# Optimization experiments

Measured on AMD Instinct MI355X. Metric: run time of the kernel, lower is better.

Reference implementation:

```python
import jax, jax.numpy as jnp
import numpy as np

EPS = 1.1920929e-07  # float32 eps, matches torch.finfo(torch.float32).eps
QMAX = 127.0         # 2**(8-1)-1 for 8-bit symmetric quantization
NUM_HEADS = 12


def _round_ste(x):
    return x + jax.lax.stop_gradient(jnp.round(x) - x)


def _floor_ste(x):
    return x + jax.lax.stop_gradient(jnp.floor(x) - x)


def _act_quant(x):
    # per-tensor symmetric 8-bit (QuantAct + SymmetricQuantFunction)
    s = jax.lax.stop_gradient(jnp.maximum(jnp.max(jnp.abs(x)) / QMAX, EPS))
    return jnp.clip(_round_ste(x / s), -QMAX - 1.0, QMAX), s


def _weight_quant(w):
    # per-output-channel symmetric 8-bit (scale.view(-1,1) path in linear_quantize)
    s = jax.lax.stop_gradient(jnp.maximum(jnp.max(jnp.abs(w), axis=1) / QMAX, EPS))
    return jnp.clip(_round_ste(w / s[:, None]), -QMAX - 1.0, QMAX), s


def _fixedpoint_requant(pre_act, pre_s, z_s):
    # fixedpoint_mul: requantize int accumulator (value pre_act on scale pre_s)
    # onto scale z_s using a 31-bit mantissa/exponent decomposition (batch_frexp).
    def int_path(pa):
        z_int = jnp.round(pa / pre_s)
        ns = pre_s / z_s
        e = jnp.floor(jnp.log2(ns)) + 1.0          # frexp exponent: ns = m * 2**e, m in [0.5,1)
        m = jnp.floor(ns * jnp.exp2(-e) * 2.0 ** 31 + 0.5)  # ROUND_HALF_UP mantissa * 2**31
        out = jnp.round(z_int * m * jnp.exp2(e - 31.0))
        return jnp.clip(out, -QMAX - 1.0, QMAX)
    hard = jax.lax.stop_gradient(int_path(pre_act))
    soft = pre_act / z_s                            # STE backward: grad / z_scaling_factor
    return soft + jax.lax.stop_gradient(hard - soft)


def _int_softmax(x_int, sf, output_bit=8, n=15):
    # IntSoftmax (shiftmax) with int_exp_shift; x_int = logits / sf (integer-valued)
    x_int = x_int - jnp.max(x_int, axis=-1, keepdims=True)
    x_int = x_int + _floor_ste(x_int / 2.0) - _floor_ste(x_int / 16.0)
    x0 = jax.lax.stop_gradient(jnp.floor(-1.0 / sf))
    x_int = jnp.maximum(x_int, n * x0)
    q = _floor_ste(x_int / x0)
    r = x_int - x0 * q
    exp_int = jnp.clip(_floor_ste((r / 2.0 - x0) * jnp.exp2(n - q)), 0.0, None)
    esum = jnp.minimum(jnp.sum(exp_int, axis=-1, keepdims=True), 2.0 ** 31 - 1.0)
    factor = _floor_ste((2.0 ** 31 - 1.0) / esum)
    exp_int = _floor_ste(exp_int * factor / 2.0 ** (31 - output_bit + 1))
    return exp_int, 1.0 / 2.0 ** (output_bit - 1)


def setup_inputs() -> dict:
    key = jax.random.key(0)
    k1, k2, k3, k4, k5 = jax.random.split(key, 5)
    B, N, C = 8, 577, 768
    return {
        "x": jax.random.normal(k1, (B, N, C), dtype=jnp.float32),
        "w_qkv": jax.random.normal(k2, (3 * C, C), dtype=jnp.float32) * 0.02,
        "b_qkv": jax.random.normal(k3, (3 * C,), dtype=jnp.float32) * 0.01,
        "w_proj": jax.random.normal(k4, (C, C), dtype=jnp.float32) * 0.02,
        "b_proj": jax.random.normal(k5, (C,), dtype=jnp.float32) * 0.01,
    }


def reference(x, w_qkv, b_qkv, w_proj, b_proj):
    B, N, C = x.shape
    H = NUM_HEADS
    D = C // H
    # ---- quantize input activation and qkv weight, integer GEMM ----
    x_int, s_x = _act_quant(x)                         # [B,N,C] int-valued, scalar scale
    wq_int, s_wq = _weight_quant(w_qkv)                # [3C,C], per-channel scale [3C]
    acc_s = s_x * s_wq                                 # accumulator scale [3C]
    qkv_int = jnp.einsum('bnc,oc->bno', x_int, wq_int) + _round_ste(b_qkv / acc_s)
    qkv_f = qkv_int * acc_s                            # dequantized qkv [B,N,3C]
    # ---- requantize qkv to per-tensor 8-bit via fixed-point mul ----
    s_qkv = jax.lax.stop_gradient(jnp.maximum(jnp.max(jnp.abs(qkv_f)) / QMAX, EPS))
    qkv8 = _fixedpoint_requant(qkv_f, acc_s, s_qkv)    # int8-valued [B,N,3C]
    qkv8 = qkv8.reshape(B, N, 3, H, D).transpose(2, 0, 3, 1, 4)
    q, k, v = qkv8[0], qkv8[1], qkv8[2]                # each [B,H,N,D]
    # ---- integer attention logits; float scale carries head_dim**-0.5 ----
    attn_int = jnp.einsum('bhnd,bhmd->bhnm', q, k)
    s_attn = s_qkv * s_qkv * (D ** -0.5)
    sm_int, s_sm = _int_softmax(attn_int, s_attn)      # int probs on scale 1/128
    # ---- integer attn @ v ----
    ctx_int = jnp.einsum('bhnm,bhmd->bhnd', sm_int, v)
    ctx_f = (ctx_int * (s_sm * s_qkv)).transpose(0, 2, 1, 3).reshape(B, N, C)
    s_ctx = jax.lax.stop_gradient(jnp.maximum(jnp.max(jnp.abs(ctx_f)) / QMAX, EPS))
    ctx8 = _fixedpoint_requant(ctx_f, s_sm * s_qkv, s_ctx)
    # ---- quantized output projection ----
    wp_int, s_wp = _weight_quant(w_proj)
    out_s = s_ctx * s_wp
    out_int = jnp.einsum('bnc,oc->bno', ctx8, wp_int) + _round_ste(b_proj / out_s)
    return out_int * out_s
```

## Files before the change

### kernel.cpp

```cpp
#include <hip/hip_runtime.h>
#include <math.h>

#define BQ 8
#define SEQ 577
#define CH 768
#define NH 12
#define HD 64
#define M_ROWS (BQ * SEQ)
#define QKV_CH (3 * CH)
#define NX (M_ROWS * CH)
#define EPSF 1.1920929e-07f
#define F2P31 2147483648.0f

#define VT_ROW 640
#define P_STRIDE 664

typedef __attribute__((ext_vector_type(4))) int i32x4;
typedef struct __align__(16) { long x, y; } L2T;

__device__ __forceinline__ void mfma_gemm_core_lds(
    const signed char* __restrict__ A, const signed char* __restrict__ Bm,
    signed char* As, signed char* Bs,
    int arow0, int bcol0, int w, int lane, i32x4 acc[4][4]) {
  int c = lane & 15, q = lane >> 4;
  int lr = lane >> 2;
  int ksb = (lane & 3) << 4;
  const signed char* Aw = As + ((w & 1) << 12);
  const signed char* Bw = Bs + ((w >> 1) << 12);
  for (int k0 = 0; k0 < CH; k0 += 64) {
#pragma unroll
    for (int u = 0; u < 2; ++u) {
      int row = (w << 5) + (u << 4) + lr;
      __builtin_amdgcn_global_load_lds(
          (const __attribute__((address_space(1))) void*)(A + (size_t)(arow0 + row) * CH + k0 + ksb),
          (__attribute__((address_space(3))) void*)(As + (w << 11) + (u << 10)),
          16, 0, 0);
      __builtin_amdgcn_global_load_lds(
          (const __attribute__((address_space(1))) void*)(Bm + (size_t)(bcol0 + row) * CH + k0 + ksb),
          (__attribute__((address_space(3))) void*)(Bs + (w << 11) + (u << 10)),
          16, 0, 0);
    }
    __syncthreads();
    L2T af[4], bf[4];
#pragma unroll
    for (int i = 0; i < 4; ++i)
      af[i] = *(const L2T*)(Aw + (((i << 4) + c) << 6) + (q << 4));
#pragma unroll
    for (int j = 0; j < 4; ++j)
      bf[j] = *(const L2T*)(Bw + (((j << 4) + c) << 6) + (q << 4));
#pragma unroll
    for (int i = 0; i < 4; ++i)
#pragma unroll
      for (int j = 0; j < 4; ++j) {
        acc[i][j] = __builtin_amdgcn_mfma_i32_16x16x32_i8(af[i].x, bf[j].x, acc[i][j], 0, 0, 0);
        acc[i][j] = __builtin_amdgcn_mfma_i32_16x16x32_i8(af[i].y, bf[j].y, acc[i][j], 0, 0, 0);
      }
    __syncthreads();
  }
}

__global__ __launch_bounds__(256) void k_prep(
    const float* __restrict__ x, const float* __restrict__ w_qkv,
    const float* __restrict__ w_proj,
    signed char* __restrict__ WQ8, float* __restrict__ SWQ,
    signed char* __restrict__ WP8, float* __restrict__ SWP,
    unsigned* __restrict__ gmax) {
  __shared__ float red[4];
  int blk = blockIdx.x, tid = threadIdx.x;
  if (blk < QKV_CH + CH) {
    const float* wr; signed char* w8; float* sw; int r;
    if (blk < QKV_CH) { r = blk; wr = w_qkv + (size_t)r * CH; w8 = WQ8 + (size_t)r * CH; sw = SWQ; }
    else { r = blk - QKV_CH; wr = w_proj + (size_t)r * CH; w8 = WP8 + (size_t)r * CH; sw = SWP; }
    float m = 0.f;
    for (int c = tid; c < CH; c += 256) m = fmaxf(m, fabsf(wr[c]));
#pragma unroll
    for (int o = 32; o; o >>= 1) m = fmaxf(m, __shfl_xor(m, o, 64));
    if ((tid & 63) == 0) red[tid >> 6] = m;
    __syncthreads();
    float mm = fmaxf(fmaxf(red[0], red[1]), fmaxf(red[2], red[3]));
    float s = fmaxf(mm / 127.0f, EPSF);
    if (tid == 0) sw[r] = s;
    for (int c = tid; c < CH; c += 256) {
      float q = rintf(wr[c] / s);
      q = fminf(fmaxf(q, -128.f), 127.f);
      w8[c] = (signed char)q;
    }
  } else {
    int ab = blk - (QKV_CH + CH);
    const float4* x4 = (const float4*)x;
    float m = 0.f;
    for (int i = ab * 256 + tid; i < NX / 4; i += 1024 * 256) {
      float4 v = x4[i];
      m = fmaxf(m, fmaxf(fmaxf(fabsf(v.x), fabsf(v.y)), fmaxf(fabsf(v.z), fabsf(v.w))));
    }
#pragma unroll
    for (int o = 32; o; o >>= 1) m = fmaxf(m, __shfl_xor(m, o, 64));
    if ((tid & 63) == 0) red[tid >> 6] = m;
    __syncthreads();
    if (tid == 0)
      atomicMax(gmax, __float_as_uint(fmaxf(fmaxf(red[0], red[1]), fmaxf(red[2], red[3]))));
  }
}

__global__ void k_aquant(const float* __restrict__ x, int n,
                         const unsigned* __restrict__ hdr, signed char* __restrict__ x8) {
  float s = fmaxf(__uint_as_float(hdr[0]) / 127.0f, EPSF);
  int n4 = n >> 2;
  const float4* x4 = (const float4*)x;
  int* dst = (int*)x8;
  int stride = gridDim.x * blockDim.x;
  for (int i = blockIdx.x * blockDim.x + threadIdx.x; i < n4; i += stride) {
    float4 v = x4[i];
    int pk = 0;
#pragma unroll
    for (int u = 0; u < 4; ++u) {
      float xv = (u == 0) ? v.x : (u == 1) ? v.y : (u == 2) ? v.z : v.w;
      float q = rintf(xv / s);
      q = fminf(fmaxf(q, -128.f), 127.f);
      pk |= ((int)(signed char)q & 0xff) << (u * 8);
    }
    dst[i] = pk;
  }
}

__global__ __launch_bounds__(256) void k_gemm_qkv(
    const signed char* __restrict__ A, const signed char* __restrict__ Bm,
    const float* __restrict__ swq, const float* __restrict__ bias,
    const unsigned* __restrict__ hdr, int* __restrict__ Cq, unsigned* __restrict__ gq) {
  __shared__ signed char As[8192], Bs[8192];
  __shared__ float red[4];
  int t = threadIdx.x;
  int lane = t & 63, w = t >> 6;
  int c = lane & 15, q = lane >> 4;
  int arow = blockIdx.y * 128 + (w & 1) * 64;
  int bcol = blockIdx.x * 128 + (w >> 1) * 64;
  i32x4 acc[4][4] = {};
  mfma_gemm_core_lds(A, Bm, As, Bs, blockIdx.y * 128, blockIdx.x * 128, w, lane, acc);
  float s_x = fmaxf(__uint_as_float(hdr[0]) / 127.0f, EPSF);
  float lmax = 0.f;
#pragma unroll
  for (int j = 0; j < 4; ++j) {
    int ccol = bcol + j * 16 + c;
    float accs = s_x * swq[ccol];
    int bint = (int)rintf(bias[ccol] / accs);
#pragma unroll
    for (int i = 0; i < 4; ++i)
#pragma unroll
      for (int r = 0; r < 4; ++r) {
        int rr = arow + i * 16 + q * 4 + r;
        if (rr < M_ROWS) {
          int qv = acc[i][j][r] + bint;
          Cq[(size_t)rr * QKV_CH + ccol] = qv;
          lmax = fmaxf(lmax, fabsf((float)qv * accs));
        }
      }
  }
#pragma unroll
  for (int off = 32; off; off >>= 1) lmax = fmaxf(lmax, __shfl_xor(lmax, off, 64));
  if (lane == 0) red[w] = lmax;
  __syncthreads();
  if (t == 0)
    atomicMax(gq, __float_as_uint(fmaxf(fmaxf(red[0], red[1]), fmaxf(red[2], red[3]))));
}

#define QK_BLKS 870
__global__ __launch_bounds__(256) void k_qkv_requant(
    const int* __restrict__ Cq, const float* __restrict__ swq,
    const unsigned* __restrict__ hdr,
    signed char* __restrict__ Q8, signed char* __restrict__ K8,
    signed char* __restrict__ VT8) {
  float s_x = fmaxf(__uint_as_float(hdr[0]) / 127.0f, EPSF);
  float s_qkv = fmaxf(__uint_as_float(hdr[1]) / 127.0f, EPSF);
  int blk = blockIdx.x, tid = threadIdx.x;
  if (blk < QK_BLKS) {
    int bx = blk % 6, by = blk / 6;
    int o = bx * 256 + tid;
    float accs = s_x * swq[o];
    float ns = accs / s_qkv;
    int e; float f = frexpf(ns, &e);
    float mm = floorf(f * F2P31 + 0.5f);
    float pw = __int_as_float((e + 96) << 23);
    int isK = (o >= CH);
    int rem = o - (isK ? CH : 0);
    int h = rem >> 6, d = rem & 63;
    signed char* dstb = isK ? K8 : Q8;
    int bn0 = by * 32;
    int bnend = min(bn0 + 32, M_ROWS);
    for (int bn = bn0; bn < bnend; ++bn) {
      int qv = Cq[(size_t)bn * QKV_CH + o];
      float qf = (float)qv * accs;
      float z = rintf(qf / accs);
      float t8 = rintf((z * mm) * pw);
      t8 = fminf(fmaxf(t8, -128.f), 127.f);
      int b = bn / SEQ, n = bn - b * SEQ;
      dstb[(((size_t)(b * NH + h) * SEQ + n) << 6) + d] = (signed char)t8;
    }
  } else {
    __shared__ signed char VTt[64 * 68];
    int vt = blk - QK_BLKS;
    int bh = vt / 10, n0 = (vt - bh * 10) * 64;
    int b = bh / NH, h = bh - b * NH;
    int od = tid & 63;
    int o = 2 * CH + h * 64 + od;
    float accs = s_x * swq[o];
    float ns = accs / s_qkv;
    int e; float f = frexpf(ns, &e);
    float mm = floorf(f * F2P31 + 0.5f);
    float pw = __int_as_float((e + 96) << 23);
    int nr = tid >> 6;
    for (int p = 0; p < 16; ++p) {
      int nl = nr * 16 + p;
      int n = n0 + nl;
      signed char v = 0;
      if (n < SEQ) {
        int qv = Cq[(size_t)(b * SEQ + n) * QKV_CH + o];
        float qf = (float)qv * accs;
        float z = rintf(qf / accs);
        float t8 = rintf((z * mm) * pw);
        t8 = fminf(fmaxf(t8, -128.f), 127.f);
        v = (signed char)t8;
      }
      VTt[od * 68 + nl] = v;
    }
    __syncthreads();
    int w16 = tid & 15, dr = tid >> 4;
#pragma unroll
    for (int pp = 0; pp < 4; ++pp) {
      int d = pp * 16 + dr;
      int val = *(const int*)&VTt[d * 68 + w16 * 4];
      *(int*)(VT8 + (size_t)bh * (64 * VT_ROW) + (size_t)d * VT_ROW + n0 + w16 * 4) = val;
    }
  }
}

__global__ __launch_bounds__(256, 4) void k_attn(
    const signed char* __restrict__ Q8, const signed char* __restrict__ K8,
    const signed char* __restrict__ VT8, const unsigned* __restrict__ hdr,
    int* __restrict__ ctxi, unsigned* __restrict__ gctx) {
  __shared__ unsigned char P[16 * P_STRIDE];
  __shared__ int Rmax[4][16];
  __shared__ unsigned long long Rsum[4][16];
  __shared__ float Rav[4];
  int tid = threadIdx.x;
  int t = tid & 63, wid = tid >> 6;
  int lin = blockIdx.x;
  int j = lin >> 3;
  int bh = (lin & 7) * 12 + j / 37;
  int qt = j % 37;
  int b = bh / NH, h = bh - b * NH;
  int col = t & 15, q4 = t >> 4;
  {
    int r = tid >> 4, w4 = tid & 15;
    *(int*)&P[r * P_STRIDE + 576 + (w4 << 2)] = 0;
  }
  const signed char* Qb = Q8 + (((size_t)bh * SEQ + qt * 16 + col) << 6);
  long qa0 = *(const long*)(Qb + q4 * 8);
  long qa1 = *(const long*)(Qb + 32 + q4 * 8);
  const signed char* Kb = K8 + ((size_t)bh * SEQ << 6);
  int kt0 = (wid == 0) ? 0 : 10 + (wid - 1) * 9;
  int ktn = (wid == 0) ? 10 : 9;
  i32x4 sv[10];
  int mx[4] = {-2147483647 - 1, -2147483647 - 1, -2147483647 - 1, -2147483647 - 1};
#pragma unroll
  for (int u = 0; u < 10; ++u) {
    if (u < ktn) {
      int kt = kt0 + u;
      const signed char* kr = Kb + ((size_t)(kt * 16 + col) << 6);
      long kb0 = *(const long*)(kr + q4 * 8);
      long kb1 = *(const long*)(kr + 32 + q4 * 8);
      i32x4 a = {0, 0, 0, 0};
      a = __builtin_amdgcn_mfma_i32_16x16x32_i8(qa0, kb0, a, 0, 0, 0);
      a = __builtin_amdgcn_mfma_i32_16x16x32_i8(qa1, kb1, a, 0, 0, 0);
      sv[u] = a;
      bool valid = (kt < 36) | (col < 1);
#pragma unroll
      for (int r = 0; r < 4; ++r)
        if (valid) mx[r] = max(mx[r], a[r]);
    }
  }
#pragma unroll
  for (int r = 0; r < 4; ++r) {
    mx[r] = max(mx[r], __shfl_xor(mx[r], 1, 64));
    mx[r] = max(mx[r], __shfl_xor(mx[r], 2, 64));
    mx[r] = max(mx[r], __shfl_xor(mx[r], 4, 64));
    mx[r] = max(mx[r], __shfl_xor(mx[r], 8, 64));
  }
  if (col == 0) {
#pragma unroll
    for (int r = 0; r < 4; ++r) Rmax[wid][q4 * 4 + r] = mx[r];
  }
  __syncthreads();
#pragma unroll
  for (int r = 0; r < 4; ++r) {
    int row = q4 * 4 + r;
    mx[r] = max(max(Rmax[0][row], Rmax[1][row]), max(Rmax[2][row], Rmax[3][row]));
  }
  float s_qkv = fmaxf(__uint_as_float(hdr[1]) / 127.0f, EPSF);
  float s_attn = (s_qkv * s_qkv) * 0.125f;
  float x0f = floorf(-1.0f / s_attn);
  int x0i = (int)x0f;
  int bi = -x0i;
  int nx0i = 15 * x0i;
  int twob = bi << 1;
  unsigned Mq = 0xFFFFFFFFu / (unsigned)bi + 1u;
  bool bOne = (Mq == 0u);
  unsigned long long su[4] = {0ull, 0ull, 0ull, 0ull};
#pragma unroll
  for (int u = 0; u < 10; ++u) {
    if (u < ktn) {
      int kt = kt0 + u;
      bool valid = (kt < 36) | (col < 1);
#pragma unroll
      for (int r = 0; r < 4; ++r) {
        int d = sv[u][r] - mx[r];
        int xi = d + (d >> 1) - (d >> 4);
        xi = max(xi, nx0i);
        xi = min(xi, 0);
        unsigned a = (unsigned)(-xi);
        unsigned q = bOne ? a : __umulhi(a, Mq);
        int rr = (int)(a - q * (unsigned)bi);
        unsigned m = (unsigned)(twob - rr);
        unsigned ue = (q < 15u) ? (m << (14 - q)) : (m >> 1);
        ue = valid ? ue : 0u;
        su[r] += ue;
        sv[u][r] = (int)ue;
      }
    }
  }
#pragma unroll
  for (int r = 0; r < 4; ++r) {
    su[r] += __shfl_xor(su[r], 1, 64);
    su[r] += __shfl_xor(su[r], 2, 64);
    su[r] += __shfl_xor(su[r], 4, 64);
    su[r] += __shfl_xor(su[r], 8, 64);
  }
  if (col == 0) {
#pragma unroll
    for (int r = 0; r < 4; ++r) Rsum[wid][q4 * 4 + r] = su[r];
  }
  __syncthreads();
  float fac[4];
#pragma unroll
  for (int r = 0; r < 4; ++r) {
    int row = q4 * 4 + r;
    unsigned long long dv = ((Rsum[0][row] + Rsum[1][row]) + Rsum[2][row]) + Rsum[3][row];
    float esum = fminf((float)dv, F2P31);
    fac[r] = floorf(F2P31 / esum);
  }
#pragma unroll
  for (int u = 0; u < 10; ++u) {
    if (u < ktn) {
      int kt = kt0 + u;
#pragma unroll
      for (int r = 0; r < 4; ++r) {
        float e = (float)(unsigned)sv[u][r];
        int p = (int)floorf((e * fac[r]) * 5.9604644775390625e-08f);
        P[(q4 * 4 + r) * P_STRIDE + kt * 16 + col] = (unsigned char)p;
      }
    }
  }
  __syncthreads();
  const signed char* Vb = VT8 + (size_t)bh * (64 * VT_ROW);
  i32x4 acc = {0, 0, 0, 0};
  for (int mc = 0; mc < 20; ++mc) {
    long pa = *(const long*)&P[col * P_STRIDE + mc * 32 + q4 * 8];
    long vb = *(const long*)(Vb + (size_t)(wid * 16 + col) * VT_ROW + mc * 32 + q4 * 8);
    acc = __builtin_amdgcn_mfma_i32_16x16x32_i8(pa, vb, acc, 0, 0, 0);
  }
  float pre_s = 0.0078125f * s_qkv;
  float avmax = 0.f;
#pragma unroll
  for (int r = 0; r < 4; ++r) {
    int n = qt * 16 + q4 * 4 + r;
    if (n < SEQ) {
      int cacc = acc[r];
      ctxi[((size_t)(b * SEQ + n)) * CH + h * 64 + wid * 16 + col] = cacc;
      avmax = fmaxf(avmax, fabsf((float)cacc * pre_s));
    }
  }
#pragma unroll
  for (int off = 32; off; off >>= 1) avmax = fmaxf(avmax, __shfl_xor(avmax, off, 64));
  if (t == 0) Rav[wid] = avmax;
  __syncthreads();
  if (tid == 0)
    atomicMax(gctx, __float_as_uint(fmaxf(fmaxf(Rav[0], Rav[1]), fmaxf(Rav[2], Rav[3]))));
}

__global__ void k_ctx_requant(const int* __restrict__ ctxi, const unsigned* __restrict__ hdr,
                              signed char* __restrict__ C8) {
  float s_qkv = fmaxf(__uint_as_float(hdr[1]) / 127.0f, EPSF);
  float pre_s = 0.0078125f * s_qkv;
  float s_ctx = fmaxf(__uint_as_float(hdr[2]) / 127.0f, EPSF);
  float ns = pre_s / s_ctx;
  int e;
  float f = frexpf(ns, &e);
  float mm = floorf(f * F2P31 + 0.5f);
  float pw = exp2f((float)e - 31.0f);
  int total4 = (M_ROWS * CH) / 4;
  int stride = gridDim.x * blockDim.x;
  const int4* src = (const int4*)ctxi;
  int* dst = (int*)C8;
  for (int i = blockIdx.x * blockDim.x + threadIdx.x; i < total4; i += stride) {
    int4 v = src[i];
    int pk = 0;
#pragma unroll
    for (int u = 0; u < 4; ++u) {
      int cv = (u == 0) ? v.x : (u == 1) ? v.y : (u == 2) ? v.z : v.w;
      float cf = (float)cv * pre_s;
      float z = rintf(cf / pre_s);
      float t8 = rintf((z * mm) * pw);
      t8 = fminf(fmaxf(t8, -128.f), 127.f);
      pk |= ((int)(signed char)t8 & 0xff) << (u * 8);
    }
    dst[i] = pk;
  }
}

__global__ __launch_bounds__(256) void k_gemm_out(
    const signed char* __restrict__ A, const signed char* __restrict__ Bm,
    const float* __restrict__ swp, const float* __restrict__ bias,
    const unsigned* __restrict__ hdr, float* __restrict__ outp) {
  __shared__ signed char As[8192], Bs[8192];
  int t = threadIdx.x;
  int lane = t & 63, w = t >> 6;
  int c = lane & 15, q = lane >> 4;
  int arow = blockIdx.y * 128 + (w & 1) * 64;
  int bcol = blockIdx.x * 128 + (w >> 1) * 64;
  i32x4 acc[4][4] = {};
  mfma_gemm_core_lds(A, Bm, As, Bs, blockIdx.y * 128, blockIdx.x * 128, w, lane, acc);
  float s_ctx = fmaxf(__uint_as_float(hdr[2]) / 127.0f, EPSF);
#pragma unroll
  for (int j = 0; j < 4; ++j) {
    int ccol = bcol + j * 16 + c;
    float outs = s_ctx * swp[ccol];
    int bint = (int)rintf(bias[ccol] / outs);
#pragma unroll
    for (int i = 0; i < 4; ++i)
#pragma unroll
      for (int r = 0; r < 4; ++r) {
        int rr = arow + i * 16 + q * 4 + r;
        if (rr < M_ROWS)
          outp[(size_t)rr * CH + ccol] = (float)(acc[i][j][r] + bint) * outs;
      }
  }
}

extern "C" void kernel_launch(void* const* d_in, const int* in_sizes, int n_in,
                              void* d_out, int out_size, void* d_ws, size_t ws_size,
                              hipStream_t stream) {
  const float* x = (const float*)d_in[0];
  const float* w_qkv = (const float*)d_in[1];
  const float* b_qkv = (const float*)d_in[2];
  const float* w_proj = (const float*)d_in[3];
  const float* b_proj = (const float*)d_in[4];
  float* outp = (float*)d_out;

  char* ws = (char*)d_ws;
  size_t off = 0;
  auto alloc = [&](size_t sz) -> char* {
    char* p = ws + off;
    off = (off + sz + 4095) & ~(size_t)4095;
    return p;
  };
  unsigned* hdr = (unsigned*)alloc(256);
  float* SWQ = (float*)alloc(QKV_CH * 4);
  float* SWP = (float*)alloc(CH * 4);
  signed char* WQ8 = (signed char*)alloc((size_t)QKV_CH * CH);
  signed char* WP8 = (signed char*)alloc((size_t)CH * CH);
  signed char* X8  = (signed char*)alloc((size_t)(M_ROWS + 128) * CH);
  signed char* Q8  = (signed char*)alloc((size_t)M_ROWS * CH);
  signed char* K8  = (signed char*)alloc((size_t)M_ROWS * CH);
  signed char* VT8 = (signed char*)alloc((size_t)BQ * NH * 64 * VT_ROW);
  signed char* C8  = (signed char*)alloc((size_t)(M_ROWS + 128) * CH);
  int* QKVI = (int*)alloc((size_t)M_ROWS * QKV_CH * 4);
  int* CTXI = (int*)alloc((size_t)M_ROWS * CH * 4);
  (void)ws_size;

  hipMemsetAsync(hdr, 0, 256, stream);
  k_prep<<<QKV_CH + CH + 1024, 256, 0, stream>>>(x, w_qkv, w_proj, WQ8, SWQ, WP8, SWP, hdr + 0);
  k_aquant<<<2048, 256, 0, stream>>>(x, NX, hdr, X8);
  dim3 g1(QKV_CH / 128, (M_ROWS + 127) / 128);
  k_gemm_qkv<<<g1, 256, 0, stream>>>(X8, WQ8, SWQ, b_qkv, hdr, QKVI, hdr + 1);
  k_qkv_requant<<<QK_BLKS + BQ * NH * 10, 256, 0, stream>>>(QKVI, SWQ, hdr, Q8, K8, VT8);
  k_attn<<<37 * BQ * NH, 256, 0, stream>>>(Q8, K8, VT8, hdr, CTXI, hdr + 2);
  k_ctx_requant<<<1024, 256, 0, stream>>>(CTXI, hdr, C8);
  dim3 g2(CH / 128, (M_ROWS + 127) / 128);
  k_gemm_out<<<g2, 256, 0, stream>>>(C8, WP8, SWP, b_proj, hdr, outp);
}
```

Before: 223.4 us.

## Use 16x16x64 int8 MFMA and spread global max atomics over slots

```diff
diff --git a/kernel.cpp b/kernel.cpp
--- a/kernel.cpp
+++ b/kernel.cpp
@@ -13,10 +13,19 @@
 #define F2P31 2147483648.0f
 
 #define VT_ROW 640
-#define P_STRIDE 664
+#define P_STRIDE 688
+
+#define NSLOT 64
+#define SLOT_STRIDE 16
 
 typedef __attribute__((ext_vector_type(4))) int i32x4;
-typedef struct __align__(16) { long x, y; } L2T;
+
+__device__ __forceinline__ float slot_scale(const unsigned* __restrict__ s) {
+  float m = 0.f;
+#pragma unroll
+  for (int i = 0; i < NSLOT; ++i) m = fmaxf(m, __uint_as_float(s[i * SLOT_STRIDE]));
+  return fmaxf(m * (1.0f / 127.0f) == 0.f ? 0.f : m / 127.0f, EPSF);
+}
 
 __device__ __forceinline__ void mfma_gemm_core_lds(
     const signed char* __restrict__ A, const signed char* __restrict__ Bm,
@@ -41,20 +50,18 @@
           16, 0, 0);
     }
     __syncthreads();
-    L2T af[4], bf[4];
+    i32x4 af[4], bf[4];
 #pragma unroll
     for (int i = 0; i < 4; ++i)
-      af[i] = *(const L2T*)(Aw + (((i << 4) + c) << 6) + (q << 4));
+      af[i] = *(const i32x4*)(Aw + (((i << 4) + c) << 6) + (q << 4));
 #pragma unroll
     for (int j = 0; j < 4; ++j)
-      bf[j] = *(const L2T*)(Bw + (((j << 4) + c) << 6) + (q << 4));
+      bf[j] = *(const i32x4*)(Bw + (((j << 4) + c) << 6) + (q << 4));
 #pragma unroll
     for (int i = 0; i < 4; ++i)
 #pragma unroll
-      for (int j = 0; j < 4; ++j) {
-        acc[i][j] = __builtin_amdgcn_mfma_i32_16x16x32_i8(af[i].x, bf[j].x, acc[i][j], 0, 0, 0);
-        acc[i][j] = __builtin_amdgcn_mfma_i32_16x16x32_i8(af[i].y, bf[j].y, acc[i][j], 0, 0, 0);
-      }
+      for (int j = 0; j < 4; ++j)
+        acc[i][j] = __builtin_amdgcn_mfma_i32_16x16x64_i8(af[i], bf[j], acc[i][j], 0, 0, 0);
     __syncthreads();
   }
 }
@@ -64,7 +71,7 @@
     const float* __restrict__ w_proj,
     signed char* __restrict__ WQ8, float* __restrict__ SWQ,
     signed char* __restrict__ WP8, float* __restrict__ SWP,
-    unsigned* __restrict__ gmax) {
+    unsigned* __restrict__ mxx) {
   __shared__ float red[4];
   int blk = blockIdx.x, tid = threadIdx.x;
   if (blk < QKV_CH + CH) {
@@ -98,13 +105,14 @@
     if ((tid & 63) == 0) red[tid >> 6] = m;
     __syncthreads();
     if (tid == 0)
-      atomicMax(gmax, __float_as_uint(fmaxf(fmaxf(red[0], red[1]), fmaxf(red[2], red[3]))));
+      atomicMax(&mxx[(ab & (NSLOT - 1)) * SLOT_STRIDE],
+                __float_as_uint(fmaxf(fmaxf(red[0], red[1]), fmaxf(red[2], red[3]))));
   }
 }
 
 __global__ void k_aquant(const float* __restrict__ x, int n,
-                         const unsigned* __restrict__ hdr, signed char* __restrict__ x8) {
-  float s = fmaxf(__uint_as_float(hdr[0]) / 127.0f, EPSF);
+                         const unsigned* __restrict__ mxx, signed char* __restrict__ x8) {
+  float s = slot_scale(mxx);
   int n4 = n >> 2;
   const float4* x4 = (const float4*)x;
   int* dst = (int*)x8;
@@ -126,7 +134,7 @@
 __global__ __launch_bounds__(256) void k_gemm_qkv(
     const signed char* __restrict__ A, const signed char* __restrict__ Bm,
     const float* __restrict__ swq, const float* __restrict__ bias,
-    const unsigned* __restrict__ hdr, int* __restrict__ Cq, unsigned* __restrict__ gq) {
+    const unsigned* __restrict__ mxx, int* __restrict__ Cq, unsigned* __restrict__ mxq) {
   __shared__ signed char As[8192], Bs[8192];
   __shared__ float red[4];
   int t = threadIdx.x;
@@ -136,7 +144,7 @@
   int bcol = blockIdx.x * 128 + (w >> 1) * 64;
   i32x4 acc[4][4] = {};
   mfma_gemm_core_lds(A, Bm, As, Bs, blockIdx.y * 128, blockIdx.x * 128, w, lane, acc);
-  float s_x = fmaxf(__uint_as_float(hdr[0]) / 127.0f, EPSF);
+  float s_x = slot_scale(mxx);
   float lmax = 0.f;
 #pragma unroll
   for (int j = 0; j < 4; ++j) {
@@ -160,17 +168,18 @@
   if (lane == 0) red[w] = lmax;
   __syncthreads();
   if (t == 0)
-    atomicMax(gq, __float_as_uint(fmaxf(fmaxf(red[0], red[1]), fmaxf(red[2], red[3]))));
+    atomicMax(&mxq[((blockIdx.y * 18 + blockIdx.x) & (NSLOT - 1)) * SLOT_STRIDE],
+              __float_as_uint(fmaxf(fmaxf(red[0], red[1]), fmaxf(red[2], red[3]))));
 }
 
 #define QK_BLKS 870
 __global__ __launch_bounds__(256) void k_qkv_requant(
     const int* __restrict__ Cq, const float* __restrict__ swq,
-    const unsigned* __restrict__ hdr,
+    const unsigned* __restrict__ mxx, const unsigned* __restrict__ mxq,
     signed char* __restrict__ Q8, signed char* __restrict__ K8,
     signed char* __restrict__ VT8) {
-  float s_x = fmaxf(__uint_as_float(hdr[0]) / 127.0f, EPSF);
-  float s_qkv = fmaxf(__uint_as_float(hdr[1]) / 127.0f, EPSF);
+  float s_x = slot_scale(mxx);
+  float s_qkv = slot_scale(mxq);
   int blk = blockIdx.x, tid = threadIdx.x;
   if (blk < QK_BLKS) {
     int bx = blk % 6, by = blk / 6;
@@ -235,8 +244,8 @@
 
 __global__ __launch_bounds__(256, 4) void k_attn(
     const signed char* __restrict__ Q8, const signed char* __restrict__ K8,
-    const signed char* __restrict__ VT8, const unsigned* __restrict__ hdr,
-    int* __restrict__ ctxi, unsigned* __restrict__ gctx) {
+    const signed char* __restrict__ VT8, const unsigned* __restrict__ mxq,
+    int* __restrict__ ctxi, unsigned* __restrict__ mxc) {
   __shared__ unsigned char P[16 * P_STRIDE];
   __shared__ int Rmax[4][16];
   __shared__ unsigned long long Rsum[4][16];
@@ -254,8 +263,7 @@
     *(int*)&P[r * P_STRIDE + 576 + (w4 << 2)] = 0;
   }
   const signed char* Qb = Q8 + (((size_t)bh * SEQ + qt * 16 + col) << 6);
-  long qa0 = *(const long*)(Qb + q4 * 8);
-  long qa1 = *(const long*)(Qb + 32 + q4 * 8);
+  i32x4 qa = *(const i32x4*)(Qb + q4 * 16);
   const signed char* Kb = K8 + ((size_t)bh * SEQ << 6);
   int kt0 = (wid == 0) ? 0 : 10 + (wid - 1) * 9;
   int ktn = (wid == 0) ? 10 : 9;
@@ -266,11 +274,9 @@
     if (u < ktn) {
       int kt = kt0 + u;
       const signed char* kr = Kb + ((size_t)(kt * 16 + col) << 6);
-      long kb0 = *(const long*)(kr + q4 * 8);
-      long kb1 = *(const long*)(kr + 32 + q4 * 8);
+      i32x4 kb = *(const i32x4*)(kr + q4 * 16);
       i32x4 a = {0, 0, 0, 0};
-      a = __builtin_amdgcn_mfma_i32_16x16x32_i8(qa0, kb0, a, 0, 0, 0);
-      a = __builtin_amdgcn_mfma_i32_16x16x32_i8(qa1, kb1, a, 0, 0, 0);
+      a = __builtin_amdgcn_mfma_i32_16x16x64_i8(qa, kb, a, 0, 0, 0);
       sv[u] = a;
       bool valid = (kt < 36) | (col < 1);
 #pragma unroll
@@ -295,7 +301,7 @@
     int row = q4 * 4 + r;
     mx[r] = max(max(Rmax[0][row], Rmax[1][row]), max(Rmax[2][row], Rmax[3][row]));
   }
-  float s_qkv = fmaxf(__uint_as_float(hdr[1]) / 127.0f, EPSF);
+  float s_qkv = slot_scale(mxq);
   float s_attn = (s_qkv * s_qkv) * 0.125f;
   float x0f = floorf(-1.0f / s_attn);
   int x0i = (int)x0f;
@@ -361,11 +367,15 @@
   }
   __syncthreads();
   const signed char* Vb = VT8 + (size_t)bh * (64 * VT_ROW);
-  i32x4 acc = {0, 0, 0, 0};
-  for (int mc = 0; mc < 20; ++mc) {
-    long pa = *(const long*)&P[col * P_STRIDE + mc * 32 + q4 * 8];
-    long vb = *(const long*)(Vb + (size_t)(wid * 16 + col) * VT_ROW + mc * 32 + q4 * 8);
-    acc = __builtin_amdgcn_mfma_i32_16x16x32_i8(pa, vb, acc, 0, 0, 0);
+  i32x4 ac0 = {0, 0, 0, 0}, ac1 = {0, 0, 0, 0};
+#pragma unroll
+  for (int mc = 0; mc < 10; mc += 2) {
+    i32x4 pa0 = *(const i32x4*)&P[col * P_STRIDE + mc * 64 + q4 * 16];
+    i32x4 vb0 = *(const i32x4*)(Vb + (size_t)(wid * 16 + col) * VT_ROW + mc * 64 + q4 * 16);
+    ac0 = __builtin_amdgcn_mfma_i32_16x16x64_i8(pa0, vb0, ac0, 0, 0, 0);
+    i32x4 pa1 = *(const i32x4*)&P[col * P_STRIDE + (mc + 1) * 64 + q4 * 16];
+    i32x4 vb1 = *(const i32x4*)(Vb + (size_t)(wid * 16 + col) * VT_ROW + (mc + 1) * 64 + q4 * 16);
+    ac1 = __builtin_amdgcn_mfma_i32_16x16x64_i8(pa1, vb1, ac1, 0, 0, 0);
   }
   float pre_s = 0.0078125f * s_qkv;
   float avmax = 0.f;
@@ -373,7 +383,7 @@
   for (int r = 0; r < 4; ++r) {
     int n = qt * 16 + q4 * 4 + r;
     if (n < SEQ) {
-      int cacc = acc[r];
+      int cacc = ac0[r] + ac1[r];
       ctxi[((size_t)(b * SEQ + n)) * CH + h * 64 + wid * 16 + col] = cacc;
       avmax = fmaxf(avmax, fabsf((float)cacc * pre_s));
     }
@@ -383,14 +393,15 @@
   if (t == 0) Rav[wid] = avmax;
   __syncthreads();
   if (tid == 0)
-    atomicMax(gctx, __float_as_uint(fmaxf(fmaxf(Rav[0], Rav[1]), fmaxf(Rav[2], Rav[3]))));
-}
-
-__global__ void k_ctx_requant(const int* __restrict__ ctxi, const unsigned* __restrict__ hdr,
-                              signed char* __restrict__ C8) {
-  float s_qkv = fmaxf(__uint_as_float(hdr[1]) / 127.0f, EPSF);
+    atomicMax(&mxc[(blockIdx.x & (NSLOT - 1)) * SLOT_STRIDE],
+              __float_as_uint(fmaxf(fmaxf(Rav[0], Rav[1]), fmaxf(Rav[2], Rav[3]))));
+}
+
+__global__ void k_ctx_requant(const int* __restrict__ ctxi, const unsigned* __restrict__ mxq,
+                              const unsigned* __restrict__ mxc, signed char* __restrict__ C8) {
+  float s_qkv = slot_scale(mxq);
   float pre_s = 0.0078125f * s_qkv;
-  float s_ctx = fmaxf(__uint_as_float(hdr[2]) / 127.0f, EPSF);
+  float s_ctx = slot_scale(mxc);
   float ns = pre_s / s_ctx;
   int e;
   float f = frexpf(ns, &e);
@@ -419,7 +430,7 @@
 __global__ __launch_bounds__(256) void k_gemm_out(
     const signed char* __restrict__ A, const signed char* __restrict__ Bm,
     const float* __restrict__ swp, const float* __restrict__ bias,
-    const unsigned* __restrict__ hdr, float* __restrict__ outp) {
+    const unsigned* __restrict__ mxc, float* __restrict__ outp) {
   __shared__ signed char As[8192], Bs[8192];
   int t = threadIdx.x;
   int lane = t & 63, w = t >> 6;
@@ -428,7 +439,7 @@
   int bcol = blockIdx.x * 128 + (w >> 1) * 64;
   i32x4 acc[4][4] = {};
   mfma_gemm_core_lds(A, Bm, As, Bs, blockIdx.y * 128, blockIdx.x * 128, w, lane, acc);
-  float s_ctx = fmaxf(__uint_as_float(hdr[2]) / 127.0f, EPSF);
+  float s_ctx = slot_scale(mxc);
 #pragma unroll
   for (int j = 0; j < 4; ++j) {
     int ccol = bcol + j * 16 + c;
@@ -462,7 +473,9 @@
     off = (off + sz + 4095) & ~(size_t)4095;
     return p;
   };
-  unsigned* hdr = (unsigned*)alloc(256);
+  unsigned* mxx = (unsigned*)alloc(3 * NSLOT * SLOT_STRIDE * 4);
+  unsigned* mxq = mxx + NSLOT * SLOT_STRIDE;
+  unsigned* mxc = mxq + NSLOT * SLOT_STRIDE;
   float* SWQ = (float*)alloc(QKV_CH * 4);
   float* SWP = (float*)alloc(CH * 4);
   signed char* WQ8 = (signed char*)alloc((size_t)QKV_CH * CH);
@@ -476,14 +489,14 @@
   int* CTXI = (int*)alloc((size_t)M_ROWS * CH * 4);
   (void)ws_size;
 
-  hipMemsetAsync(hdr, 0, 256, stream);
-  k_prep<<<QKV_CH + CH + 1024, 256, 0, stream>>>(x, w_qkv, w_proj, WQ8, SWQ, WP8, SWP, hdr + 0);
-  k_aquant<<<2048, 256, 0, stream>>>(x, NX, hdr, X8);
+  hipMemsetAsync(mxx, 0, 3 * NSLOT * SLOT_STRIDE * 4, stream);
+  k_prep<<<QKV_CH + CH + 1024, 256, 0, stream>>>(x, w_qkv, w_proj, WQ8, SWQ, WP8, SWP, mxx);
+  k_aquant<<<2048, 256, 0, stream>>>(x, NX, mxx, X8);
   dim3 g1(QKV_CH / 128, (M_ROWS + 127) / 128);
-  k_gemm_qkv<<<g1, 256, 0, stream>>>(X8, WQ8, SWQ, b_qkv, hdr, QKVI, hdr + 1);
-  k_qkv_requant<<<QK_BLKS + BQ * NH * 10, 256, 0, stream>>>(QKVI, SWQ, hdr, Q8, K8, VT8);
-  k_attn<<<37 * BQ * NH, 256, 0, stream>>>(Q8, K8, VT8, hdr, CTXI, hdr + 2);
-  k_ctx_requant<<<1024, 256, 0, stream>>>(CTXI, hdr, C8);
+  k_gemm_qkv<<<g1, 256, 0, stream>>>(X8, WQ8, SWQ, b_qkv, mxx, QKVI, mxq);
+  k_qkv_requant<<<QK_BLKS + BQ * NH * 10, 256, 0, stream>>>(QKVI, SWQ, mxx, mxq, Q8, K8, VT8);
+  k_attn<<<37 * BQ * NH, 256, 0, stream>>>(Q8, K8, VT8, mxq, CTXI, mxc);
+  k_ctx_requant<<<1024, 256, 0, stream>>>(CTXI, mxq, mxc, C8);
   dim3 g2(CH / 128, (M_ROWS + 127) / 128);
-  k_gemm_out<<<g2, 256, 0, stream>>>(C8, WP8, SWP, b_proj, hdr, outp);
-}
+  k_gemm_out<<<g2, 256, 0, stream>>>(C8, WP8, SWP, b_proj, mxc, outp);
+}
```

Measured after the change: 200.8 us. 1.11x faster.
